# Performance work log

Measured on AMD Instinct MI355X. Metric: run time of the kernel, lower is better.

Reference implementation:

```python
import jax, jax.numpy as jnp
import numpy as np

N = 100000      # n_nodes
D = 64          # in_features (= out_features)
H = 4           # attention heads
DK = D // H     # per-head dim
E = 1600000     # num edges (avg degree 16)
STEP = 0.25     # ODE euler step size
NSTEPS = 4      # integrate t in [0, 1]
ALPHA = 0.2     # LeakyReLU negative slope


def setup_inputs() -> dict:
    key = jax.random.key(0)
    k1, k2, k3, k4 = jax.random.split(key, 4)
    x = jax.random.normal(k1, (N, D), dtype=jnp.float32)
    edge_index = jax.random.randint(k2, (2, E), 0, N, dtype=jnp.int32)
    edge_weight = jax.random.uniform(k3, (E,), dtype=jnp.float32)
    # HamAgg.weight: init.eye_ -> identity [D, D]
    W = jnp.eye(D, dtype=jnp.float32)
    # HAM_GATConv.a: xavier_normal_ on shape (2*d_k, 1, 1), gain=1.414
    a = jax.random.normal(k4, (2 * DK,), dtype=jnp.float32) * (1.414 * np.sqrt(2.0 / (2 * DK + 1)))
    return {"x": x, "edge_index": edge_index, "edge_weight": edge_weight, "W": W, "a": a}


def reference(x, edge_index, edge_weight, W, a):
    # ---- Hamiltonian ODE block (args.vt == 'fc', odemap 'h1extend') ----
    # xt = hstack([x, x @ W.T]); euler-integrate canonical Hamiltonian flow
    # dq/dt = p, dp/dt = -q over t in [0,1] with step 0.25; keep first D dims.
    q = x
    p = x @ W.T
    for _ in range(NSTEPS):
        q, p = q + STEP * p, p - STEP * q
    xt = q  # out_x = out[..., :D]

    row, col = edge_index[0], edge_index[1]

    # ---- HAM_GATConv attention (W_x = x @ I = x) ----
    # h[n, head, k] = xt[n, head*DK + k]
    h = xt.reshape(N, H, DK)
    a_src, a_dst = a[:DK], a[DK:]
    s_src = h @ a_src   # [N, H] per-node source contribution
    s_dst = h @ a_dst   # [N, H] per-node dest contribution
    score = jax.nn.leaky_relu(s_src[row] + s_dst[col], ALPHA)  # [E, H]

    # segment softmax grouped by destination (edge[1])
    seg_max = jax.ops.segment_max(score, col, num_segments=N)  # [N, H]
    seg_max = jnp.where(jnp.isfinite(seg_max), seg_max, 0.0)
    e = jnp.exp(score - seg_max[col])
    denom = jax.ops.segment_sum(e, col, num_segments=N)
    att = e / (denom[col] + 1e-16)  # [E, H]

    # ---- mean over heads of per-head spmm == single spmm with mean attention ----
    # spmm: out[row[e]] += att[e] * xt[col[e]]
    w = att.mean(axis=1)  # [E]
    out = jax.ops.segment_sum(w[:, None] * xt[col], row, num_segments=N)  # [N, D]
    return out
```

## Files before the change

### kernel.cpp

```cpp
#include <hip/hip_runtime.h>
#include <hip/hip_bf16.h>


#define LRELU(v) ((v) > 0.0f ? (v) : 0.2f * (v))

#define EC 4096
#define BSC 256
#define BSR 128
#define NPW 8
#define NPB 32

__device__ __forceinline__ float bf16_to_f32(unsigned short u) {
    return __uint_as_float((unsigned int)u << 16);
}
__device__ __forceinline__ unsigned short f32_to_bf16(float f) {
    __hip_bfloat16 h = __float2bfloat16(f);
    return *reinterpret_cast<unsigned short*>(&h);
}

__global__ __launch_bounds__(256) void k_node(const float* __restrict__ x,
                                              const float* __restrict__ W,
                                              const float* __restrict__ a,
                                              unsigned short* __restrict__ xt16,
                                              float* __restrict__ s_src,
                                              float* __restrict__ s_dst,
                                              int n, float c1, float c2) {
    __shared__ float Ws[64 * 68];
    __shared__ float xs[NPB * 64];
    int t = threadIdx.x;
    for (int i = t; i < 64 * 64; i += 256)
        Ws[(i >> 6) * 68 + (i & 63)] = W[i];
    {
        size_t gbase = (size_t)blockIdx.x * NPB * 64;
        for (int i = t; i < NPB * 64; i += 256) {
            size_t g = gbase + i;
            xs[i] = (g < (size_t)n * 64) ? x[g] : 0.0f;
        }
    }
    __syncthreads();
    int wave = t >> 6;
    int lane = t & 63;
    float a_s = a[lane & 15];
    float a_d = a[16 + (lane & 15)];
    int nbase = blockIdx.x * NPB + wave * NPW;
    const float* xw = xs + wave * NPW * 64;

    float p[NPW];
#pragma unroll
    for (int j = 0; j < NPW; ++j) p[j] = 0.0f;

#pragma unroll 2
    for (int k4 = 0; k4 < 64; k4 += 4) {
        float4 wr = *(const float4*)(Ws + lane * 68 + k4);
#pragma unroll
        for (int j = 0; j < NPW; ++j) {
            float4 xb = *(const float4*)(xw + j * 64 + k4);
            p[j] = fmaf(xb.x, wr.x, p[j]);
            p[j] = fmaf(xb.y, wr.y, p[j]);
            p[j] = fmaf(xb.z, wr.z, p[j]);
            p[j] = fmaf(xb.w, wr.w, p[j]);
        }
    }

#pragma unroll
    for (int j = 0; j < NPW; ++j) {
        int node = nbase + j;
        if (node < n) {
            float xv = xw[j * 64 + lane];
            float xtv = c1 * xv + c2 * p[j];
            xt16[(size_t)node * 64 + lane] = f32_to_bf16(xtv);
            float ss = xtv * a_s;
            float sd = xtv * a_d;
#pragma unroll
            for (int off = 8; off >= 1; off >>= 1) {
                ss += __shfl_xor(ss, off, 64);
                sd += __shfl_xor(sd, off, 64);
            }
            if ((lane & 15) == 0) {
                int h = lane >> 4;
                s_src[node * 4 + h] = ss;
                s_dst[node * 4 + h] = sd;
            }
        }
    }
}

__global__ __launch_bounds__(256) void k_hist(const int* __restrict__ row,
                                              const int* __restrict__ col,
                                              int* __restrict__ Hr,
                                              int* __restrict__ Hc,
                                              int e, int nblk, int nbr, int nbc) {
    __shared__ int hr[1024];
    __shared__ int hc[512];
    int t = threadIdx.x;
    for (int i = t; i < 1024; i += 256) hr[i] = 0;
    for (int i = t; i < 512; i += 256) hc[i] = 0;
    __syncthreads();
    int base = blockIdx.x * EC;
#pragma unroll
    for (int j = 0; j < EC / 256; ++j) {
        int i = base + t + j * 256;
        if (i < e) {
            atomicAdd(&hr[row[i] >> 7], 1);
            atomicAdd(&hc[col[i] >> 8], 1);
        }
    }
    __syncthreads();
    for (int b = t; b < nbr; b += 256) Hr[(size_t)b * nblk + blockIdx.x] = hr[b];
    for (int b = t; b < nbc; b += 256) Hc[(size_t)b * nblk + blockIdx.x] = hc[b];
}

__global__ __launch_bounds__(256) void k_scanH2(int* __restrict__ Hr,
                                                int* __restrict__ Hc,
                                                int* __restrict__ BtotR,
                                                int* __restrict__ BtotC,
                                                int nblk, int nbr) {
    __shared__ int vals[512];
    __shared__ int part[256];
    int t = threadIdx.x;
    int bb = blockIdx.x;
    int* Hb;
    int* Btot;
    if (bb < nbr) {
        Hb = Hr + (size_t)bb * nblk;
        Btot = BtotR + bb;
    } else {
        Hb = Hc + (size_t)(bb - nbr) * nblk;
        Btot = BtotC + (bb - nbr);
    }
    for (int i = t; i < nblk; i += 256) vals[i] = Hb[i];
    __syncthreads();
    int c0 = t * 2;
    int s = 0;
#pragma unroll
    for (int j = 0; j < 2; ++j)
        if (c0 + j < nblk) s += vals[c0 + j];
    part[t] = s;
    __syncthreads();
    for (int d = 1; d < 256; d <<= 1) {
        int add = (t >= d) ? part[t - d] : 0;
        __syncthreads();
        part[t] += add;
        __syncthreads();
    }
    int run = part[t] - s;
#pragma unroll
    for (int j = 0; j < 2; ++j) {
        int i = c0 + j;
        if (i < nblk) {
            int v = vals[i];
            Hb[i] = run;
            run += v;
        }
    }
    if (t == 255) *Btot = part[255];
}

__global__ __launch_bounds__(256) void k_base2(const int* __restrict__ BtotR,
                                               int* __restrict__ BbR, int nbr,
                                               const int* __restrict__ BtotC,
                                               int* __restrict__ BbC, int nbc) {
    const int* Btot = (blockIdx.x == 0) ? BtotR : BtotC;
    int* Bbase = (blockIdx.x == 0) ? BbR : BbC;
    int nb = (blockIdx.x == 0) ? nbr : nbc;
    __shared__ int part[256];
    __shared__ int carry;
    int t = threadIdx.x;
    if (t == 0) carry = 0;
    __syncthreads();
    for (int base = 0; base < nb; base += 256) {
        int i = base + t;
        int v = (i < nb) ? Btot[i] : 0;
        part[t] = v;
        __syncthreads();
        for (int d = 1; d < 256; d <<= 1) {
            int add = (t >= d) ? part[t - d] : 0;
            __syncthreads();
            part[t] += add;
            __syncthreads();
        }
        if (i < nb) Bbase[i] = carry + part[t] - v;
        __syncthreads();
        if (t == 0) carry += part[255];
        __syncthreads();
    }
    if (t == 0) Bbase[nb] = carry;
}

__global__ __launch_bounds__(256) void k_scatter_dual(
    const int* __restrict__ row, const int* __restrict__ col,
    const int* __restrict__ Hr, const int* __restrict__ Hc,
    const int* __restrict__ BbR, const int* __restrict__ BbC,
    int* __restrict__ ebr, int* __restrict__ ebc,
    int e, int nblk, int nbr, int nbc) {
    __shared__ int curr[1024];
    __shared__ int curc[512];
    int t = threadIdx.x;
    int blk = blockIdx.x;
    for (int b = t; b < nbr; b += 256) curr[b] = BbR[b] + Hr[(size_t)b * nblk + blk];
    for (int b = t; b < nbc; b += 256) curc[b] = BbC[b] + Hc[(size_t)b * nblk + blk];
    __syncthreads();
    int base = blk * EC;
#pragma unroll
    for (int j = 0; j < EC / 256; ++j) {
        int i = base + t + j * 256;
        if (i < e) {
            int r = row[i], c = col[i];
            int pr = atomicAdd(&curr[r >> 7], 1);
            ebr[pr] = (c << 7) | (r & 127);
            int pc = atomicAdd(&curc[c >> 8], 1);
            ebc[pc] = (r << 8) | (c & 255);
        }
    }
}

__global__ __launch_bounds__(256) void k_denom_b(const int* __restrict__ ebc,
                                                 const int* __restrict__ BbC,
                                                 const float* __restrict__ s_src,
                                                 const float* __restrict__ s_dst,
                                                 float* __restrict__ rden, int n) {
    __shared__ float acc[BSC * 4];
    __shared__ float sd[BSC * 4];
    int t = threadIdx.x;
    int b = blockIdx.x;
    int cbase = b << 8;
    for (int i = t; i < BSC * 4; i += 256) {
        acc[i] = 0.0f;
        int c4 = cbase * 4 + i;
        sd[i] = (c4 < n * 4) ? s_dst[c4] : 0.0f;
    }
    __syncthreads();
    int start = BbC[b], end = BbC[b + 1];
    for (int i = start + t; i < end; i += 256) {
        int p = ebc[i];
        int r = p >> 8, cl = p & 255;
        float4 ss = *(const float4*)(s_src + (size_t)r * 4);
        atomicAdd(&acc[cl * 4 + 0], __expf(LRELU(ss.x + sd[cl * 4 + 0])));
        atomicAdd(&acc[cl * 4 + 1], __expf(LRELU(ss.y + sd[cl * 4 + 1])));
        atomicAdd(&acc[cl * 4 + 2], __expf(LRELU(ss.z + sd[cl * 4 + 2])));
        atomicAdd(&acc[cl * 4 + 3], __expf(LRELU(ss.w + sd[cl * 4 + 3])));
    }
    __syncthreads();
    for (int i = t; i < BSC * 4; i += 256) {
        int c4 = cbase * 4 + i;
        if (c4 < n * 4) rden[c4] = 1.0f / (acc[i] + 1e-16f);
    }
}

__global__ __launch_bounds__(256) void k_sort2(const int* __restrict__ ebr,
                                               const int* __restrict__ BbR,
                                               const float* __restrict__ s_src,
                                               const float* __restrict__ s_dst,
                                               const float* __restrict__ rden,
                                               int* __restrict__ rowptr,
                                               int* __restrict__ cw_c,
                                               float* __restrict__ cw_w,
                                               int n, int e) {
    __shared__ int cnt[BSR];
    __shared__ int pfx[BSR];
    __shared__ int cur[BSR];
    __shared__ float ssh[BSR * 4];
    int t = threadIdx.x;
    int b = blockIdx.x;
    int rbase = b << 7;
    if (t < BSR) cnt[t] = 0;
    for (int i = t; i < BSR * 4; i += 256) {
        int g = rbase * 4 + i;
        ssh[i] = (g < n * 4) ? s_src[g] : 0.0f;
    }
    __syncthreads();
    int start = BbR[b], end = BbR[b + 1];
    for (int i = start + t; i < end; i += 256)
        atomicAdd(&cnt[ebr[i] & 127], 1);
    __syncthreads();
    if (t < BSR) pfx[t] = cnt[t];
    __syncthreads();
    for (int d = 1; d < BSR; d <<= 1) {
        int v = (t < BSR && t >= d) ? pfx[t - d] : 0;
        __syncthreads();
        if (t < BSR) pfx[t] += v;
        __syncthreads();
    }
    if (t < BSR) {
        int excl = start + pfx[t] - cnt[t];
        cur[t] = excl;
        int r = rbase + t;
        if (r < n) rowptr[r] = excl;
    }
    if (b == 0 && t == 0) rowptr[n] = e;
    __syncthreads();
    for (int i = start + t; i < end; i += 256) {
        int p = ebr[i];
        int rl = p & 127, c = p >> 7;
        float4 sd = *(const float4*)(s_dst + (size_t)c * 4);
        float4 rd = *(const float4*)(rden + (size_t)c * 4);
        float wv = __expf(LRELU(ssh[rl * 4 + 0] + sd.x)) * rd.x +
                   __expf(LRELU(ssh[rl * 4 + 1] + sd.y)) * rd.y +
                   __expf(LRELU(ssh[rl * 4 + 2] + sd.z)) * rd.z +
                   __expf(LRELU(ssh[rl * 4 + 3] + sd.w)) * rd.w;
        int pos = atomicAdd(&cur[rl], 1);
        cw_c[pos] = c;
        cw_w[pos] = 0.25f * wv;
    }
}

__global__ __launch_bounds__(256) void k_aggr(const int* __restrict__ rowptr,
                                              const int* __restrict__ cw_c,
                                              const float* __restrict__ cw_w,
                                              const unsigned short* __restrict__ xt16,
                                              float* __restrict__ out, int n) {
    int r = blockIdx.x * 4 + (threadIdx.x >> 6);
    if (r >= n) return;
    int lane = threadIdx.x & 63;
    int start = rowptr[r], end = rowptr[r + 1];
    float acc = 0.0f;
    for (int base = start; base < end; base += 64) {
        int m = min(64, end - base);
        int cc = 0;
        float ww = 0.0f;
        if (lane < m) {
            cc = cw_c[base + lane];
            ww = cw_w[base + lane];
        }
        int k = 0;
        for (; k + 8 <= m; k += 8) {
            int c0 = __shfl(cc, k + 0, 64), c1 = __shfl(cc, k + 1, 64);
            int c2 = __shfl(cc, k + 2, 64), c3 = __shfl(cc, k + 3, 64);
            int c4 = __shfl(cc, k + 4, 64), c5 = __shfl(cc, k + 5, 64);
            int c6 = __shfl(cc, k + 6, 64), c7 = __shfl(cc, k + 7, 64);
            float w0 = __shfl(ww, k + 0, 64), w1 = __shfl(ww, k + 1, 64);
            float w2 = __shfl(ww, k + 2, 64), w3 = __shfl(ww, k + 3, 64);
            float w4 = __shfl(ww, k + 4, 64), w5 = __shfl(ww, k + 5, 64);
            float w6 = __shfl(ww, k + 6, 64), w7 = __shfl(ww, k + 7, 64);
            unsigned short u0 = xt16[(size_t)c0 * 64 + lane];
            unsigned short u1 = xt16[(size_t)c1 * 64 + lane];
            unsigned short u2 = xt16[(size_t)c2 * 64 + lane];
            unsigned short u3 = xt16[(size_t)c3 * 64 + lane];
            unsigned short u4 = xt16[(size_t)c4 * 64 + lane];
            unsigned short u5 = xt16[(size_t)c5 * 64 + lane];
            unsigned short u6 = xt16[(size_t)c6 * 64 + lane];
            unsigned short u7 = xt16[(size_t)c7 * 64 + lane];
            acc = fmaf(w0, bf16_to_f32(u0), acc);
            acc = fmaf(w1, bf16_to_f32(u1), acc);
            acc = fmaf(w2, bf16_to_f32(u2), acc);
            acc = fmaf(w3, bf16_to_f32(u3), acc);
            acc = fmaf(w4, bf16_to_f32(u4), acc);
            acc = fmaf(w5, bf16_to_f32(u5), acc);
            acc = fmaf(w6, bf16_to_f32(u6), acc);
            acc = fmaf(w7, bf16_to_f32(u7), acc);
        }
        for (; k < m; ++k) {
            int c0 = __shfl(cc, k, 64);
            float w0 = __shfl(ww, k, 64);
            acc = fmaf(w0, bf16_to_f32(xt16[(size_t)c0 * 64 + lane]), acc);
        }
    }
    out[(size_t)r * 64 + lane] = acc;
}

extern "C" void kernel_launch(void* const* d_in, const int* in_sizes, int n_in,
                              void* d_out, int out_size, void* d_ws, size_t ws_size,
                              hipStream_t stream) {
    const float* x = (const float*)d_in[0];
    const int* ei = (const int*)d_in[1];
    const float* W = (const float*)d_in[3];
    const float* a = (const float*)d_in[4];
    int n = in_sizes[0] / 64;
    int e = in_sizes[1] / 2;
    const int* row = ei;
    const int* col = ei + e;
    float* out = (float*)d_out;

    int nblk = (e + EC - 1) / EC;
    int nbr = (n + BSR - 1) / BSR;
    int nbc = (n + BSC - 1) / BSC;

    size_t o = 0;
    auto take = [&](size_t cnt) {
        size_t p = o;
        o += (cnt + 3) & ~(size_t)3;
        return p;
    };
    int* wsi = (int*)d_ws;
    unsigned short* xt16 = (unsigned short*)(wsi + take((size_t)n * 32));
    float* s_src = (float*)(wsi + take((size_t)n * 4));
    float* s_dst = (float*)(wsi + take((size_t)n * 4));
    float* rden = (float*)(wsi + take((size_t)n * 4));
    int* Hr = wsi + take((size_t)nbr * nblk);
    int* Hc = wsi + take((size_t)nbc * nblk);
    int* BtotR = wsi + take(nbr);
    int* BbR = wsi + take(nbr + 1);
    int* BtotC = wsi + take(nbc);
    int* BbC = wsi + take(nbc + 1);
    int* ebr = wsi + take(e);
    int* ebc = wsi + take(e);
    float* cw_w = (float*)(wsi + take(e));
    int* rowptr = wsi + take(n + 1);
    int* cw_c = ebc;

    float aq = 1.f, bq = 0.f, ap = 0.f, bp = 1.f;
    for (int i = 0; i < 4; ++i) {
        float naq = aq + 0.25f * ap, nbq = bq + 0.25f * bp;
        float nap = ap - 0.25f * aq, nbp = bp - 0.25f * bq;
        aq = naq; bq = nbq; ap = nap; bp = nbp;
    }

    k_node<<<(n + NPB - 1) / NPB, 256, 0, stream>>>(x, W, a, xt16, s_src, s_dst,
                                                    n, aq, bq);
    k_hist<<<nblk, 256, 0, stream>>>(row, col, Hr, Hc, e, nblk, nbr, nbc);
    k_scanH2<<<nbr + nbc, 256, 0, stream>>>(Hr, Hc, BtotR, BtotC, nblk, nbr);
    k_base2<<<2, 256, 0, stream>>>(BtotR, BbR, nbr, BtotC, BbC, nbc);
    k_scatter_dual<<<nblk, 256, 0, stream>>>(row, col, Hr, Hc, BbR, BbC,
                                             ebr, ebc, e, nblk, nbr, nbc);
    k_denom_b<<<nbc, 256, 0, stream>>>(ebc, BbC, s_src, s_dst, rden, n);
    k_sort2<<<nbr, 256, 0, stream>>>(ebr, BbR, s_src, s_dst, rden,
                                     rowptr, cw_c, cw_w, n, e);
    k_aggr<<<(n + 3) / 4, 256, 0, stream>>>(rowptr, cw_c, cw_w, xt16, out, n);
}
```

Baseline: 325.1 us.

## Fuse row sort and aggregation into bucketed LDS-atomic accumulation kernel

Removes the per-row sort kernel (k_sort2) and the separate CSR aggregation kernel. A single kernel now processes each 64-row bucket: it computes attention weights in chunks into shared memory, gathers bf16 xt rows and accumulates into a 64x64 LDS tile with shared atomics. The row bucket size drops from 128 to 64 so the tile fits in LDS, which doubles the histogram and scatter bucket counts. This saves writing and re-reading the cw arrays and one launch, but adds LDS atomic contention and gives only about 1560 blocks, so parallelism is lower.

```diff
diff --git a/kernel.cpp b/kernel.cpp
--- a/kernel.cpp
+++ b/kernel.cpp
@@ -6,9 +6,10 @@
 
 #define EC 4096
 #define BSC 256
-#define BSR 128
+#define BSR 64
 #define NPW 8
 #define NPB 32
+#define CH 1024
 
 __device__ __forceinline__ float bf16_to_f32(unsigned short u) {
     return __uint_as_float((unsigned int)u << 16);
@@ -90,10 +91,10 @@
                                               int* __restrict__ Hr,
                                               int* __restrict__ Hc,
                                               int e, int nblk, int nbr, int nbc) {
-    __shared__ int hr[1024];
+    __shared__ int hr[2048];
     __shared__ int hc[512];
     int t = threadIdx.x;
-    for (int i = t; i < 1024; i += 256) hr[i] = 0;
+    for (int i = t; i < 2048; i += 256) hr[i] = 0;
     for (int i = t; i < 512; i += 256) hc[i] = 0;
     __syncthreads();
     int base = blockIdx.x * EC;
@@ -101,7 +102,7 @@
     for (int j = 0; j < EC / 256; ++j) {
         int i = base + t + j * 256;
         if (i < e) {
-            atomicAdd(&hr[row[i] >> 7], 1);
+            atomicAdd(&hr[row[i] >> 6], 1);
             atomicAdd(&hc[col[i] >> 8], 1);
         }
     }
@@ -193,7 +194,7 @@
     const int* __restrict__ BbR, const int* __restrict__ BbC,
     int* __restrict__ ebr, int* __restrict__ ebc,
     int e, int nblk, int nbr, int nbc) {
-    __shared__ int curr[1024];
+    __shared__ int curr[2048];
     __shared__ int curc[512];
     int t = threadIdx.x;
     int blk = blockIdx.x;
@@ -206,8 +207,8 @@
         int i = base + t + j * 256;
         if (i < e) {
             int r = row[i], c = col[i];
-            int pr = atomicAdd(&curr[r >> 7], 1);
-            ebr[pr] = (c << 7) | (r & 127);
+            int pr = atomicAdd(&curr[r >> 6], 1);
+            ebr[pr] = (c << 6) | (r & 63);
             int pc = atomicAdd(&curc[c >> 8], 1);
             ebc[pc] = (r << 8) | (c & 255);
         }
@@ -247,115 +248,68 @@
     }
 }
 
-__global__ __launch_bounds__(256) void k_sort2(const int* __restrict__ ebr,
-                                               const int* __restrict__ BbR,
-                                               const float* __restrict__ s_src,
-                                               const float* __restrict__ s_dst,
-                                               const float* __restrict__ rden,
-                                               int* __restrict__ rowptr,
-                                               int* __restrict__ cw_c,
-                                               float* __restrict__ cw_w,
-                                               int n, int e) {
-    __shared__ int cnt[BSR];
-    __shared__ int pfx[BSR];
-    __shared__ int cur[BSR];
+__global__ __launch_bounds__(256) void k_aggr_b(const int* __restrict__ ebr,
+                                                const int* __restrict__ BbR,
+                                                const float* __restrict__ s_src,
+                                                const float* __restrict__ s_dst,
+                                                const float* __restrict__ rden,
+                                                const unsigned short* __restrict__ xt16,
+                                                float* __restrict__ out, int n) {
+    __shared__ float acc[BSR * 64];
     __shared__ float ssh[BSR * 4];
+    __shared__ float wsh[CH];
+    __shared__ int psh[CH];
     int t = threadIdx.x;
     int b = blockIdx.x;
-    int rbase = b << 7;
-    if (t < BSR) cnt[t] = 0;
+    int rbase = b << 6;
+    for (int i = t; i < BSR * 64; i += 256) acc[i] = 0.0f;
     for (int i = t; i < BSR * 4; i += 256) {
         int g = rbase * 4 + i;
         ssh[i] = (g < n * 4) ? s_src[g] : 0.0f;
     }
     __syncthreads();
     int start = BbR[b], end = BbR[b + 1];
-    for (int i = start + t; i < end; i += 256)
-        atomicAdd(&cnt[ebr[i] & 127], 1);
-    __syncthreads();
-    if (t < BSR) pfx[t] = cnt[t];
-    __syncthreads();
-    for (int d = 1; d < BSR; d <<= 1) {
-        int v = (t < BSR && t >= d) ? pfx[t - d] : 0;
-        __syncthreads();
-        if (t < BSR) pfx[t] += v;
-        __syncthreads();
-    }
-    if (t < BSR) {
-        int excl = start + pfx[t] - cnt[t];
-        cur[t] = excl;
-        int r = rbase + t;
-        if (r < n) rowptr[r] = excl;
-    }
-    if (b == 0 && t == 0) rowptr[n] = e;
-    __syncthreads();
-    for (int i = start + t; i < end; i += 256) {
-        int p = ebr[i];
-        int rl = p & 127, c = p >> 7;
-        float4 sd = *(const float4*)(s_dst + (size_t)c * 4);
-        float4 rd = *(const float4*)(rden + (size_t)c * 4);
-        float wv = __expf(LRELU(ssh[rl * 4 + 0] + sd.x)) * rd.x +
-                   __expf(LRELU(ssh[rl * 4 + 1] + sd.y)) * rd.y +
-                   __expf(LRELU(ssh[rl * 4 + 2] + sd.z)) * rd.z +
-                   __expf(LRELU(ssh[rl * 4 + 3] + sd.w)) * rd.w;
-        int pos = atomicAdd(&cur[rl], 1);
-        cw_c[pos] = c;
-        cw_w[pos] = 0.25f * wv;
-    }
-}
-
-__global__ __launch_bounds__(256) void k_aggr(const int* __restrict__ rowptr,
-                                              const int* __restrict__ cw_c,
-                                              const float* __restrict__ cw_w,
-                                              const unsigned short* __restrict__ xt16,
-                                              float* __restrict__ out, int n) {
-    int r = blockIdx.x * 4 + (threadIdx.x >> 6);
-    if (r >= n) return;
-    int lane = threadIdx.x & 63;
-    int start = rowptr[r], end = rowptr[r + 1];
-    float acc = 0.0f;
-    for (int base = start; base < end; base += 64) {
-        int m = min(64, end - base);
-        int cc = 0;
-        float ww = 0.0f;
-        if (lane < m) {
-            cc = cw_c[base + lane];
-            ww = cw_w[base + lane];
-        }
-        int k = 0;
-        for (; k + 8 <= m; k += 8) {
-            int c0 = __shfl(cc, k + 0, 64), c1 = __shfl(cc, k + 1, 64);
-            int c2 = __shfl(cc, k + 2, 64), c3 = __shfl(cc, k + 3, 64);
-            int c4 = __shfl(cc, k + 4, 64), c5 = __shfl(cc, k + 5, 64);
-            int c6 = __shfl(cc, k + 6, 64), c7 = __shfl(cc, k + 7, 64);
-            float w0 = __shfl(ww, k + 0, 64), w1 = __shfl(ww, k + 1, 64);
-            float w2 = __shfl(ww, k + 2, 64), w3 = __shfl(ww, k + 3, 64);
-            float w4 = __shfl(ww, k + 4, 64), w5 = __shfl(ww, k + 5, 64);
-            float w6 = __shfl(ww, k + 6, 64), w7 = __shfl(ww, k + 7, 64);
-            unsigned short u0 = xt16[(size_t)c0 * 64 + lane];
-            unsigned short u1 = xt16[(size_t)c1 * 64 + lane];
-            unsigned short u2 = xt16[(size_t)c2 * 64 + lane];
-            unsigned short u3 = xt16[(size_t)c3 * 64 + lane];
-            unsigned short u4 = xt16[(size_t)c4 * 64 + lane];
-            unsigned short u5 = xt16[(size_t)c5 * 64 + lane];
-            unsigned short u6 = xt16[(size_t)c6 * 64 + lane];
-            unsigned short u7 = xt16[(size_t)c7 * 64 + lane];
-            acc = fmaf(w0, bf16_to_f32(u0), acc);
-            acc = fmaf(w1, bf16_to_f32(u1), acc);
-            acc = fmaf(w2, bf16_to_f32(u2), acc);
-            acc = fmaf(w3, bf16_to_f32(u3), acc);
-            acc = fmaf(w4, bf16_to_f32(u4), acc);
-            acc = fmaf(w5, bf16_to_f32(u5), acc);
-            acc = fmaf(w6, bf16_to_f32(u6), acc);
-            acc = fmaf(w7, bf16_to_f32(u7), acc);
-        }
-        for (; k < m; ++k) {
-            int c0 = __shfl(cc, k, 64);
-            float w0 = __shfl(ww, k, 64);
-            acc = fmaf(w0, bf16_to_f32(xt16[(size_t)c0 * 64 + lane]), acc);
-        }
-    }
-    out[(size_t)r * 64 + lane] = acc;
+    int wave = t >> 6, lane = t & 63;
+    for (int chunk = start; chunk < end; chunk += CH) {
+        int cend = min(end, chunk + CH);
+        for (int i = chunk + t; i < cend; i += 256) {
+            int p = ebr[i];
+            int rl = p & 63, c = p >> 6;
+            float4 sd = *(const float4*)(s_dst + (size_t)c * 4);
+            float4 rd = *(const float4*)(rden + (size_t)c * 4);
+            float wv = __expf(LRELU(ssh[rl * 4 + 0] + sd.x)) * rd.x +
+                       __expf(LRELU(ssh[rl * 4 + 1] + sd.y)) * rd.y +
+                       __expf(LRELU(ssh[rl * 4 + 2] + sd.z)) * rd.z +
+                       __expf(LRELU(ssh[rl * 4 + 3] + sd.w)) * rd.w;
+            wsh[i - chunk] = 0.25f * wv;
+            psh[i - chunk] = p;
+        }
+        __syncthreads();
+        for (int i0 = chunk + wave * 8; i0 < cend; i0 += 32) {
+            int pj[8];
+            float pw[8];
+            unsigned short u[8];
+#pragma unroll
+            for (int j = 0; j < 8; ++j) {
+                int i = i0 + j;
+                bool v = (i < cend);
+                pj[j] = v ? psh[i - chunk] : 0;
+                pw[j] = v ? wsh[i - chunk] : 0.0f;
+            }
+#pragma unroll
+            for (int j = 0; j < 8; ++j)
+                u[j] = xt16[(size_t)(pj[j] >> 6) * 64 + lane];
+#pragma unroll
+            for (int j = 0; j < 8; ++j)
+                atomicAdd(&acc[(pj[j] & 63) * 64 + lane],
+                          pw[j] * bf16_to_f32(u[j]));
+        }
+        __syncthreads();
+    }
+    for (int i = t; i < BSR * 64; i += 256) {
+        int r = rbase + (i >> 6);
+        if (r < n) out[(size_t)r * 64 + (i & 63)] = acc[i];
+    }
 }
 
 extern "C" void kernel_launch(void* const* d_in, const int* in_sizes, int n_in,
@@ -394,9 +348,6 @@
     int* BbC = wsi + take(nbc + 1);
     int* ebr = wsi + take(e);
     int* ebc = wsi + take(e);
-    float* cw_w = (float*)(wsi + take(e));
-    int* rowptr = wsi + take(n + 1);
-    int* cw_c = ebc;
 
     float aq = 1.f, bq = 0.f, ap = 0.f, bp = 1.f;
     for (int i = 0; i < 4; ++i) {
@@ -413,7 +364,6 @@
     k_scatter_dual<<<nblk, 256, 0, stream>>>(row, col, Hr, Hc, BbR, BbC,
                                              ebr, ebc, e, nblk, nbr, nbc);
     k_denom_b<<<nbc, 256, 0, stream>>>(ebc, BbC, s_src, s_dst, rden, n);
-    k_sort2<<<nbr, 256, 0, stream>>>(ebr, BbR, s_src, s_dst, rden,
-                                     rowptr, cw_c, cw_w, n, e);
-    k_aggr<<<(n + 3) / 4, 256, 0, stream>>>(rowptr, cw_c, cw_w, xt16, out, n);
-}
+    k_aggr_b<<<nbr, 256, 0, stream>>>(ebr, BbR, s_src, s_dst, rden,
+                                      xt16, out, n);
+}
```

New measurement: 860.4 us. 2.65x slower.

## Pack column and weight pairs and vectorize aggregation across lane groups

Applied to the files above, without the earlier changes.

The sort kernel now writes each edge's column index and attention weight as a single int2, so the aggregation kernel needs one load per edge instead of two. The aggregation kernel splits each wavefront into four 16-lane groups. Each group handles a different edge, each lane loads four bf16 features with ushort4, up to eight edges are kept in flight per lane, and the groups' partial sums are combined with xor shuffles at the end. The goal is more memory-level parallelism and wider gathers, at the cost of a final shuffle reduction, idle slots on low-degree rows, and reusing the ebc workspace as the packed buffer.

```diff
diff --git a/kernel.cpp b/kernel.cpp
--- a/kernel.cpp
+++ b/kernel.cpp
@@ -253,8 +253,7 @@
                                                const float* __restrict__ s_dst,
                                                const float* __restrict__ rden,
                                                int* __restrict__ rowptr,
-                                               int* __restrict__ cw_c,
-                                               float* __restrict__ cw_w,
+                                               int2* __restrict__ cwp,
                                                int n, int e) {
     __shared__ int cnt[BSR];
     __shared__ int pfx[BSR];
@@ -299,63 +298,57 @@
                    __expf(LRELU(ssh[rl * 4 + 2] + sd.z)) * rd.z +
                    __expf(LRELU(ssh[rl * 4 + 3] + sd.w)) * rd.w;
         int pos = atomicAdd(&cur[rl], 1);
-        cw_c[pos] = c;
-        cw_w[pos] = 0.25f * wv;
+        cwp[pos] = make_int2(c, __float_as_int(0.25f * wv));
     }
 }
 
 __global__ __launch_bounds__(256) void k_aggr(const int* __restrict__ rowptr,
-                                              const int* __restrict__ cw_c,
-                                              const float* __restrict__ cw_w,
+                                              const int2* __restrict__ cwp,
                                               const unsigned short* __restrict__ xt16,
-                                              float* __restrict__ out, int n) {
+                                              float* __restrict__ out, int n, int e) {
     int r = blockIdx.x * 4 + (threadIdx.x >> 6);
     if (r >= n) return;
     int lane = threadIdx.x & 63;
+    int g = lane >> 4;
+    int l = lane & 15;
     int start = rowptr[r], end = rowptr[r + 1];
-    float acc = 0.0f;
-    for (int base = start; base < end; base += 64) {
-        int m = min(64, end - base);
-        int cc = 0;
-        float ww = 0.0f;
-        if (lane < m) {
-            cc = cw_c[base + lane];
-            ww = cw_w[base + lane];
-        }
-        int k = 0;
-        for (; k + 8 <= m; k += 8) {
-            int c0 = __shfl(cc, k + 0, 64), c1 = __shfl(cc, k + 1, 64);
-            int c2 = __shfl(cc, k + 2, 64), c3 = __shfl(cc, k + 3, 64);
-            int c4 = __shfl(cc, k + 4, 64), c5 = __shfl(cc, k + 5, 64);
-            int c6 = __shfl(cc, k + 6, 64), c7 = __shfl(cc, k + 7, 64);
-            float w0 = __shfl(ww, k + 0, 64), w1 = __shfl(ww, k + 1, 64);
-            float w2 = __shfl(ww, k + 2, 64), w3 = __shfl(ww, k + 3, 64);
-            float w4 = __shfl(ww, k + 4, 64), w5 = __shfl(ww, k + 5, 64);
-            float w6 = __shfl(ww, k + 6, 64), w7 = __shfl(ww, k + 7, 64);
-            unsigned short u0 = xt16[(size_t)c0 * 64 + lane];
-            unsigned short u1 = xt16[(size_t)c1 * 64 + lane];
-            unsigned short u2 = xt16[(size_t)c2 * 64 + lane];
-            unsigned short u3 = xt16[(size_t)c3 * 64 + lane];
-            unsigned short u4 = xt16[(size_t)c4 * 64 + lane];
-            unsigned short u5 = xt16[(size_t)c5 * 64 + lane];
-            unsigned short u6 = xt16[(size_t)c6 * 64 + lane];
-            unsigned short u7 = xt16[(size_t)c7 * 64 + lane];
-            acc = fmaf(w0, bf16_to_f32(u0), acc);
-            acc = fmaf(w1, bf16_to_f32(u1), acc);
-            acc = fmaf(w2, bf16_to_f32(u2), acc);
-            acc = fmaf(w3, bf16_to_f32(u3), acc);
-            acc = fmaf(w4, bf16_to_f32(u4), acc);
-            acc = fmaf(w5, bf16_to_f32(u5), acc);
-            acc = fmaf(w6, bf16_to_f32(u6), acc);
-            acc = fmaf(w7, bf16_to_f32(u7), acc);
-        }
-        for (; k < m; ++k) {
-            int c0 = __shfl(cc, k, 64);
-            float w0 = __shfl(ww, k, 64);
-            acc = fmaf(w0, bf16_to_f32(xt16[(size_t)c0 * 64 + lane]), acc);
-        }
-    }
-    out[(size_t)r * 64 + lane] = acc;
+    float4 acc = {0.0f, 0.0f, 0.0f, 0.0f};
+    for (int base = start; base < end; base += 32) {
+        int m = end - base;
+        if (m > 32) m = 32;
+        int nk = (m + 3) >> 2;
+        ushort4 u[8];
+        float wv[8];
+#pragma unroll
+        for (int k = 0; k < 8; ++k) {
+            if (k < nk) {
+                int idx = base + k * 4 + g;
+                int idc = idx < e ? idx : e - 1;
+                int2 cw = cwp[idc];
+                wv[k] = (idx < end) ? __int_as_float(cw.y) : 0.0f;
+                u[k] = *(const ushort4*)(xt16 + (size_t)cw.x * 64 + l * 4);
+            } else {
+                wv[k] = 0.0f;
+                u[k] = make_ushort4(0, 0, 0, 0);
+            }
+        }
+#pragma unroll
+        for (int k = 0; k < 8; ++k) {
+            acc.x = fmaf(wv[k], bf16_to_f32(u[k].x), acc.x);
+            acc.y = fmaf(wv[k], bf16_to_f32(u[k].y), acc.y);
+            acc.z = fmaf(wv[k], bf16_to_f32(u[k].z), acc.z);
+            acc.w = fmaf(wv[k], bf16_to_f32(u[k].w), acc.w);
+        }
+    }
+    acc.x += __shfl_xor(acc.x, 16, 64);
+    acc.y += __shfl_xor(acc.y, 16, 64);
+    acc.z += __shfl_xor(acc.z, 16, 64);
+    acc.w += __shfl_xor(acc.w, 16, 64);
+    acc.x += __shfl_xor(acc.x, 32, 64);
+    acc.y += __shfl_xor(acc.y, 32, 64);
+    acc.z += __shfl_xor(acc.z, 32, 64);
+    acc.w += __shfl_xor(acc.w, 32, 64);
+    if (lane < 16) *(float4*)(out + (size_t)r * 64 + l * 4) = acc;
 }
 
 extern "C" void kernel_launch(void* const* d_in, const int* in_sizes, int n_in,
@@ -393,10 +386,10 @@
     int* BtotC = wsi + take(nbc);
     int* BbC = wsi + take(nbc + 1);
     int* ebr = wsi + take(e);
-    int* ebc = wsi + take(e);
-    float* cw_w = (float*)(wsi + take(e));
+    int* cwbuf = wsi + take((size_t)2 * e);
+    int* ebc = cwbuf;
+    int2* cwp = (int2*)cwbuf;
     int* rowptr = wsi + take(n + 1);
-    int* cw_c = ebc;
 
     float aq = 1.f, bq = 0.f, ap = 0.f, bp = 1.f;
     for (int i = 0; i < 4; ++i) {
@@ -414,6 +407,6 @@
                                              ebr, ebc, e, nblk, nbr, nbc);
     k_denom_b<<<nbc, 256, 0, stream>>>(ebc, BbC, s_src, s_dst, rden, n);
     k_sort2<<<nbr, 256, 0, stream>>>(ebr, BbR, s_src, s_dst, rden,
-                                     rowptr, cw_c, cw_w, n, e);
-    k_aggr<<<(n + 3) / 4, 256, 0, stream>>>(rowptr, cw_c, cw_w, xt16, out, n);
-}
+                                     rowptr, cwp, n, e);
+    k_aggr<<<(n + 3) / 4, 256, 0, stream>>>(rowptr, cwp, xt16, out, n, e);
+}
```

Result: faster. 310.9 us (-4.4%).
